# Optimization experiments

Hardware: AMD Instinct MI355X
Metric: run time of the kernel (lower is better)

Reference implementation:

```python
import jax, jax.numpy as jnp
import numpy as np

NUM_NODES = 10000
NUM_EDGES = 640000
IN_FEAT = 128
OUT_FEAT = 128


def setup_inputs() -> dict:
    key = jax.random.key(0)
    k_x, k_e, k_w = jax.random.split(key, 3)
    x = jax.random.normal(k_x, (NUM_NODES, IN_FEAT), dtype=jnp.float32)
    edge_index = jax.random.randint(k_e, (2, NUM_EDGES), 0, NUM_NODES, dtype=jnp.int64)
    # Xavier-uniform W, zeros B (as in the torch init)
    limit = float(np.sqrt(6.0 / (IN_FEAT + OUT_FEAT)))
    W = jax.random.uniform(k_w, (OUT_FEAT, IN_FEAT), dtype=jnp.float32, minval=-limit, maxval=limit)
    B = jnp.zeros((OUT_FEAT, IN_FEAT), dtype=jnp.float32)
    return {"x": x, "edge_index": edge_index, "W": W, "B": B}


def reference(x, edge_index, W, B):
    num_nodes = x.shape[0]
    src, dst = edge_index[0], edge_index[1]
    # gather messages from source nodes, scatter-add into destination nodes
    messages = x[src]  # [num_edges, in_feat]
    agg = jax.ops.segment_sum(messages, dst, num_segments=num_nodes)  # [num_nodes, in_feat]
    # in-degree normalization (zero-degree nodes -> divide by 1)
    deg = jax.ops.segment_sum(jnp.ones_like(dst, dtype=x.dtype), dst, num_segments=num_nodes)
    deg = jnp.where(deg == 0, jnp.asarray(1.0, x.dtype), deg)
    agg = agg / deg[:, None]
    # dual linear combine: messages @ W.T + x @ B.T
    return agg @ W.T + x @ B.T
```

## Files before the change

### kernel.cpp

```cpp
#include <hip/hip_runtime.h>

#define NUM_NODES 10000
#define NUM_EDGES 640000
#define FEAT 128
#define K2 256
#define NPB 64
#define NBUCK 157
#define BCAP 6144
#define DEG_MAX 128

using bf16x8 = __attribute__((ext_vector_type(8))) short;
using f32x4 = __attribute__((ext_vector_type(4))) float;

static __device__ inline unsigned short f2bf(float f) {
  union { float f; unsigned int u; } v;
  v.f = f;
  unsigned int r = v.u + 0x7FFF + ((v.u >> 16) & 1);
  return (unsigned short)(r >> 16);
}
static __device__ inline float bf2f(unsigned short u) {
  union { unsigned int u; float f; } v;
  v.u = ((unsigned int)u) << 16;
  return v.f;
}

__global__ __launch_bounds__(256) void convert_bin_kernel(
    const float* __restrict__ x,
    const float* __restrict__ W,
    const float* __restrict__ B,
    const int* __restrict__ src,
    const int* __restrict__ dst,
    unsigned short* __restrict__ Xbf,
    unsigned short* __restrict__ Bbuf,
    unsigned int* __restrict__ staging,
    int* __restrict__ bucket_cnt) {
  __shared__ int hist[NBUCK];
  __shared__ int wbase[NBUCK];
  int blk = blockIdx.x;
  int tid = threadIdx.x;
  if (blk < 1250) {
    int base = (blk * 256 + tid) * 4;
    float4 v = *(const float4*)(x + base);
    ushort4 o;
    o.x = f2bf(v.x); o.y = f2bf(v.y); o.z = f2bf(v.z); o.w = f2bf(v.w);
    *(ushort4*)(Xbf + base) = o;
  } else if (blk < 1282) {
    int base = ((blk - 1250) * 256 + tid) * 4;
    const float* srcp;
    size_t dstoff;
    if (base < FEAT * FEAT) {
      int o = base >> 7, k = base & 127;
      srcp = W + base;
      dstoff = (size_t)o * K2 + k;
    } else {
      int b = base - FEAT * FEAT;
      int o = b >> 7, k = b & 127;
      srcp = B + b;
      dstoff = (size_t)o * K2 + FEAT + k;
    }
    float4 v = *(const float4*)srcp;
    ushort4 ov;
    ov.x = f2bf(v.x); ov.y = f2bf(v.y); ov.z = f2bf(v.z); ov.w = f2bf(v.w);
    *(ushort4*)(Bbuf + dstoff) = ov;
  } else {
    int ebase = (blk - 1282) * 1024;
    for (int t = tid; t < NBUCK; t += 256) hist[t] = 0;
    __syncthreads();
    int s[4], d[4], bkt[4];
#pragma unroll
    for (int i = 0; i < 4; ++i) {
      int e = ebase + tid + i * 256;
      s[i] = src[e];
      d[i] = dst[e];
      bkt[i] = d[i] >> 6;
      atomicAdd(&hist[bkt[i]], 1);
    }
    __syncthreads();
    for (int t = tid; t < NBUCK; t += 256) {
      wbase[t] = atomicAdd(&bucket_cnt[t], hist[t]);
      hist[t] = 0;
    }
    __syncthreads();
#pragma unroll
    for (int i = 0; i < 4; ++i) {
      int r = atomicAdd(&hist[bkt[i]], 1);
      int off = wbase[bkt[i]] + r;
      if (off < BCAP)
        staging[(size_t)bkt[i] * BCAP + off] =
            ((unsigned int)(d[i] & 63) << 16) | (unsigned int)s[i];
    }
  }
}

__global__ __launch_bounds__(1024) void aggregate_kernel(
    const unsigned int* __restrict__ staging,
    const int* __restrict__ bucket_cnt,
    const unsigned short* __restrict__ Xbf,
    unsigned short* __restrict__ Aggbf) {
  __shared__ unsigned short lcsr[NPB * DEG_MAX];
  __shared__ int lcnt[NPB];
  int b = blockIdx.x;
  int tid = threadIdx.x;
  if (tid < NPB) lcnt[tid] = 0;
  __syncthreads();
  int nb = bucket_cnt[b];
  if (nb > BCAP) nb = BCAP;
  const unsigned int* st = staging + (size_t)b * BCAP;
  for (int i = tid; i < nb; i += 1024) {
    unsigned int e = st[i];
    int dl = e >> 16;
    int pos = atomicAdd(&lcnt[dl], 1);
    if (pos < DEG_MAX) lcsr[dl * DEG_MAX + pos] = (unsigned short)(e & 0xFFFF);
  }
  __syncthreads();

  int grp = tid >> 5;
  int lane = tid & 31;
#pragma unroll
  for (int it = 0; it < 2; ++it) {
    int nl = it * 32 + grp;
    int node = b * NPB + nl;
    if (node >= NUM_NODES) continue;
    int deg = lcnt[nl];
    if (deg > DEG_MAX) deg = DEG_MAX;
    const unsigned short* row = lcsr + nl * DEG_MAX;
    float a0[4] = {0.f, 0.f, 0.f, 0.f};
    float a1[4] = {0.f, 0.f, 0.f, 0.f};
    float a2[4] = {0.f, 0.f, 0.f, 0.f};
    float a3[4] = {0.f, 0.f, 0.f, 0.f};
    int e = 0;
    for (; e + 4 <= deg; e += 4) {
      int s0 = row[e], s1 = row[e + 1], s2 = row[e + 2], s3 = row[e + 3];
      ushort4 v0 = *(const ushort4*)(Xbf + (size_t)s0 * FEAT + lane * 4);
      ushort4 v1 = *(const ushort4*)(Xbf + (size_t)s1 * FEAT + lane * 4);
      ushort4 v2 = *(const ushort4*)(Xbf + (size_t)s2 * FEAT + lane * 4);
      ushort4 v3 = *(const ushort4*)(Xbf + (size_t)s3 * FEAT + lane * 4);
      a0[0] += bf2f(v0.x); a0[1] += bf2f(v0.y); a0[2] += bf2f(v0.z); a0[3] += bf2f(v0.w);
      a1[0] += bf2f(v1.x); a1[1] += bf2f(v1.y); a1[2] += bf2f(v1.z); a1[3] += bf2f(v1.w);
      a2[0] += bf2f(v2.x); a2[1] += bf2f(v2.y); a2[2] += bf2f(v2.z); a2[3] += bf2f(v2.w);
      a3[0] += bf2f(v3.x); a3[1] += bf2f(v3.y); a3[2] += bf2f(v3.z); a3[3] += bf2f(v3.w);
    }
    for (; e < deg; ++e) {
      int s0 = row[e];
      ushort4 v0 = *(const ushort4*)(Xbf + (size_t)s0 * FEAT + lane * 4);
      a0[0] += bf2f(v0.x); a0[1] += bf2f(v0.y); a0[2] += bf2f(v0.z); a0[3] += bf2f(v0.w);
    }
    float sc = (deg == 0) ? 1.0f : (1.0f / (float)deg);
    ushort4 o;
    o.x = f2bf((a0[0] + a1[0] + a2[0] + a3[0]) * sc);
    o.y = f2bf((a0[1] + a1[1] + a2[1] + a3[1]) * sc);
    o.z = f2bf((a0[2] + a1[2] + a2[2] + a3[2]) * sc);
    o.w = f2bf((a0[3] + a1[3] + a2[3] + a3[3]) * sc);
    *(ushort4*)(Aggbf + (size_t)node * FEAT + lane * 4) = o;
  }
}

__global__ __launch_bounds__(64) void gemm_kernel(
    const unsigned short* __restrict__ Aggbf,
    const unsigned short* __restrict__ Xbf,
    const unsigned short* __restrict__ Bbuf,
    float* __restrict__ out) {
  int l = threadIdx.x;
  int r = l & 15;
  int g = l >> 4;
  int rowbase = blockIdx.x * 16;
  int arow = rowbase + r;

  f32x4 acc[8] = {};
#pragma unroll
  for (int ks = 0; ks < 8; ++ks) {
    const unsigned short* Ab = (ks < 4)
        ? (Aggbf + (size_t)arow * FEAT + ks * 32)
        : (Xbf + (size_t)arow * FEAT + (ks - 4) * 32);
    bf16x8 a = *(const bf16x8*)(Ab + g * 8);
    int kb = ks * 32 + g * 8;
#pragma unroll
    for (int nt = 0; nt < 8; ++nt) {
      bf16x8 b = *(const bf16x8*)(Bbuf + (size_t)(nt * 16 + r) * K2 + kb);
      acc[nt] = __builtin_amdgcn_mfma_f32_16x16x32_bf16(a, b, acc[nt], 0, 0, 0);
    }
  }

#pragma unroll
  for (int nt = 0; nt < 8; ++nt) {
#pragma unroll
    for (int j = 0; j < 4; ++j) {
      int rr = rowbase + g * 4 + j;
      out[(size_t)rr * FEAT + nt * 16 + r] = acc[nt][j];
    }
  }
}

extern "C" void kernel_launch(void* const* d_in, const int* in_sizes, int n_in,
                              void* d_out, int out_size, void* d_ws, size_t ws_size,
                              hipStream_t stream) {
  const float* x = (const float*)d_in[0];
  const int* ei = (const int*)d_in[1];
  const float* W = (const float*)d_in[2];
  const float* B = (const float*)d_in[3];
  float* out = (float*)d_out;

  unsigned short* Xbf = (unsigned short*)d_ws;
  unsigned short* Aggbf = Xbf + (size_t)NUM_NODES * FEAT;
  unsigned short* Bbuf = Aggbf + (size_t)NUM_NODES * FEAT;
  unsigned int* staging = (unsigned int*)(Bbuf + (size_t)FEAT * K2);
  int* bucket_cnt = (int*)(staging + (size_t)NBUCK * BCAP);

  const int* src = ei;
  const int* dst = ei + NUM_EDGES;

  hipMemsetAsync(bucket_cnt, 0, NBUCK * sizeof(int), stream);

  convert_bin_kernel<<<1907, 256, 0, stream>>>(x, W, B, src, dst, Xbf, Bbuf,
                                               staging, bucket_cnt);
  aggregate_kernel<<<NBUCK, 1024, 0, stream>>>(staging, bucket_cnt, Xbf, Aggbf);
  gemm_kernel<<<NUM_NODES / 16, 64, 0, stream>>>(Aggbf, Xbf, Bbuf, out);
}
```

Before: 115.9 us.

## Fuse aggregation with MFMA GEMM and use smaller 32-node buckets

Merges the aggregation and GEMM kernels into one. Each block aggregates 32 nodes into a padded shared-memory tile and then runs the bf16 MFMA GEMM straight from LDS, so the global Aggbf round-trip and one kernel launch go away. The buckets shrink to 32 nodes, which doubles the number of blocks to 313 for better CU occupancy, and each binning block now processes 4096 edges to cut global atomics. The tradeoff is lower per-block parallelism in the GEMM phase and bucket capacity limits that could drop edges if they overflow.

```diff
diff --git a/kernel.cpp b/kernel.cpp
--- a/kernel.cpp
+++ b/kernel.cpp
@@ -4,10 +4,11 @@
 #define NUM_EDGES 640000
 #define FEAT 128
 #define K2 256
-#define NPB 64
-#define NBUCK 157
-#define BCAP 6144
+#define NPB 32
+#define NBUCK 313
+#define BCAP 2560
 #define DEG_MAX 128
+#define ASTRIDE 136
 
 using bf16x8 = __attribute__((ext_vector_type(8))) short;
 using f32x4 = __attribute__((ext_vector_type(4))) float;
@@ -63,17 +64,21 @@
     ov.x = f2bf(v.x); ov.y = f2bf(v.y); ov.z = f2bf(v.z); ov.w = f2bf(v.w);
     *(ushort4*)(Bbuf + dstoff) = ov;
   } else {
-    int ebase = (blk - 1282) * 1024;
+    int ebase = (blk - 1282) * 4096;
     for (int t = tid; t < NBUCK; t += 256) hist[t] = 0;
     __syncthreads();
-    int s[4], d[4], bkt[4];
-#pragma unroll
-    for (int i = 0; i < 4; ++i) {
+    int s[16], d[16];
+#pragma unroll
+    for (int i = 0; i < 16; ++i) {
       int e = ebase + tid + i * 256;
-      s[i] = src[e];
-      d[i] = dst[e];
-      bkt[i] = d[i] >> 6;
-      atomicAdd(&hist[bkt[i]], 1);
+      if (e < NUM_EDGES) {
+        s[i] = src[e];
+        d[i] = dst[e];
+        atomicAdd(&hist[d[i] >> 5], 1);
+      } else {
+        s[i] = -1;
+        d[i] = 0;
+      }
     }
     __syncthreads();
     for (int t = tid; t < NBUCK; t += 256) {
@@ -82,23 +87,28 @@
     }
     __syncthreads();
 #pragma unroll
-    for (int i = 0; i < 4; ++i) {
-      int r = atomicAdd(&hist[bkt[i]], 1);
-      int off = wbase[bkt[i]] + r;
-      if (off < BCAP)
-        staging[(size_t)bkt[i] * BCAP + off] =
-            ((unsigned int)(d[i] & 63) << 16) | (unsigned int)s[i];
-    }
-  }
-}
-
-__global__ __launch_bounds__(1024) void aggregate_kernel(
+    for (int i = 0; i < 16; ++i) {
+      if (s[i] >= 0) {
+        int bkt = d[i] >> 5;
+        int r = atomicAdd(&hist[bkt], 1);
+        int off = wbase[bkt] + r;
+        if (off < BCAP)
+          staging[(size_t)bkt * BCAP + off] =
+              ((unsigned int)(d[i] & 31) << 16) | (unsigned int)s[i];
+      }
+    }
+  }
+}
+
+__global__ __launch_bounds__(512) void agg_gemm_kernel(
     const unsigned int* __restrict__ staging,
     const int* __restrict__ bucket_cnt,
     const unsigned short* __restrict__ Xbf,
-    unsigned short* __restrict__ Aggbf) {
+    const unsigned short* __restrict__ Bbuf,
+    float* __restrict__ out) {
   __shared__ unsigned short lcsr[NPB * DEG_MAX];
   __shared__ int lcnt[NPB];
+  __shared__ __attribute__((aligned(16))) unsigned short aggA[NPB * ASTRIDE];
   int b = blockIdx.x;
   int tid = threadIdx.x;
   if (tid < NPB) lcnt[tid] = 0;
@@ -106,7 +116,7 @@
   int nb = bucket_cnt[b];
   if (nb > BCAP) nb = BCAP;
   const unsigned int* st = staging + (size_t)b * BCAP;
-  for (int i = tid; i < nb; i += 1024) {
+  for (int i = tid; i < nb; i += 512) {
     unsigned int e = st[i];
     int dl = e >> 16;
     int pos = atomicAdd(&lcnt[dl], 1);
@@ -118,10 +128,8 @@
   int lane = tid & 31;
 #pragma unroll
   for (int it = 0; it < 2; ++it) {
-    int nl = it * 32 + grp;
-    int node = b * NPB + nl;
-    if (node >= NUM_NODES) continue;
-    int deg = lcnt[nl];
+    int nl = it * 16 + grp;
+    int deg = (b * NPB + nl < NUM_NODES) ? lcnt[nl] : 0;
     if (deg > DEG_MAX) deg = DEG_MAX;
     const unsigned short* row = lcsr + nl * DEG_MAX;
     float a0[4] = {0.f, 0.f, 0.f, 0.f};
@@ -151,42 +159,41 @@
     o.y = f2bf((a0[1] + a1[1] + a2[1] + a3[1]) * sc);
     o.z = f2bf((a0[2] + a1[2] + a2[2] + a3[2]) * sc);
     o.w = f2bf((a0[3] + a1[3] + a2[3] + a3[3]) * sc);
-    *(ushort4*)(Aggbf + (size_t)node * FEAT + lane * 4) = o;
-  }
-}
-
-__global__ __launch_bounds__(64) void gemm_kernel(
-    const unsigned short* __restrict__ Aggbf,
-    const unsigned short* __restrict__ Xbf,
-    const unsigned short* __restrict__ Bbuf,
-    float* __restrict__ out) {
-  int l = threadIdx.x;
+    *(ushort4*)(aggA + nl * ASTRIDE + lane * 4) = o;
+  }
+  __syncthreads();
+
+  int w = tid >> 6;
+  int l = tid & 63;
   int r = l & 15;
   int g = l >> 4;
-  int rowbase = blockIdx.x * 16;
-  int arow = rowbase + r;
-
-  f32x4 acc[8] = {};
+  int rt = w >> 2;
+  int ct0 = w & 3;
+  int arl = rt * 16 + r;
+  int arg = b * NPB + arl;
+  if (arg >= NUM_NODES) arg = NUM_NODES - 1;
+
+  f32x4 acc0 = {}, acc1 = {};
 #pragma unroll
   for (int ks = 0; ks < 8; ++ks) {
-    const unsigned short* Ab = (ks < 4)
-        ? (Aggbf + (size_t)arow * FEAT + ks * 32)
-        : (Xbf + (size_t)arow * FEAT + (ks - 4) * 32);
-    bf16x8 a = *(const bf16x8*)(Ab + g * 8);
+    bf16x8 a;
+    if (ks < 4)
+      a = *(const bf16x8*)(aggA + arl * ASTRIDE + ks * 32 + g * 8);
+    else
+      a = *(const bf16x8*)(Xbf + (size_t)arg * FEAT + (ks - 4) * 32 + g * 8);
     int kb = ks * 32 + g * 8;
-#pragma unroll
-    for (int nt = 0; nt < 8; ++nt) {
-      bf16x8 b = *(const bf16x8*)(Bbuf + (size_t)(nt * 16 + r) * K2 + kb);
-      acc[nt] = __builtin_amdgcn_mfma_f32_16x16x32_bf16(a, b, acc[nt], 0, 0, 0);
-    }
-  }
-
-#pragma unroll
-  for (int nt = 0; nt < 8; ++nt) {
-#pragma unroll
-    for (int j = 0; j < 4; ++j) {
-      int rr = rowbase + g * 4 + j;
-      out[(size_t)rr * FEAT + nt * 16 + r] = acc[nt][j];
+    bf16x8 b0 = *(const bf16x8*)(Bbuf + (size_t)(ct0 * 16 + r) * K2 + kb);
+    bf16x8 b1 = *(const bf16x8*)(Bbuf + (size_t)((ct0 + 4) * 16 + r) * K2 + kb);
+    acc0 = __builtin_amdgcn_mfma_f32_16x16x32_bf16(a, b0, acc0, 0, 0, 0);
+    acc1 = __builtin_amdgcn_mfma_f32_16x16x32_bf16(a, b1, acc1, 0, 0, 0);
+  }
+
+#pragma unroll
+  for (int j = 0; j < 4; ++j) {
+    int rr = b * NPB + rt * 16 + g * 4 + j;
+    if (rr < NUM_NODES) {
+      out[(size_t)rr * FEAT + ct0 * 16 + r] = acc0[j];
+      out[(size_t)rr * FEAT + (ct0 + 4) * 16 + r] = acc1[j];
     }
   }
 }
@@ -201,8 +208,7 @@
   float* out = (float*)d_out;
 
   unsigned short* Xbf = (unsigned short*)d_ws;
-  unsigned short* Aggbf = Xbf + (size_t)NUM_NODES * FEAT;
-  unsigned short* Bbuf = Aggbf + (size_t)NUM_NODES * FEAT;
+  unsigned short* Bbuf = Xbf + (size_t)NUM_NODES * FEAT;
   unsigned int* staging = (unsigned int*)(Bbuf + (size_t)FEAT * K2);
   int* bucket_cnt = (int*)(staging + (size_t)NBUCK * BCAP);
 
@@ -211,8 +217,8 @@
 
   hipMemsetAsync(bucket_cnt, 0, NBUCK * sizeof(int), stream);
 
-  convert_bin_kernel<<<1907, 256, 0, stream>>>(x, W, B, src, dst, Xbf, Bbuf,
+  convert_bin_kernel<<<1439, 256, 0, stream>>>(x, W, B, src, dst, Xbf, Bbuf,
                                                staging, bucket_cnt);
-  aggregate_kernel<<<NBUCK, 1024, 0, stream>>>(staging, bucket_cnt, Xbf, Aggbf);
-  gemm_kernel<<<NUM_NODES / 16, 64, 0, stream>>>(Aggbf, Xbf, Bbuf, out);
-}
+  agg_gemm_kernel<<<NBUCK, 512, 0, stream>>>(staging, bucket_cnt, Xbf, Bbuf,
+                                             out);
+}
```

After: 111.7 us. -3.6%, faster.
